# Kernel optimization log

Hardware: AMD Instinct MI355X
Metric: run time of the kernel (lower is better)

## Reference

```python
import math
import jax, jax.numpy as jnp
import numpy as np

B, CIN, COUT, K, Z, H, W = 8, 512, 512, 3, 512, 64, 64


def setup_inputs() -> dict:
    key = jax.random.key(0)
    k1, k2, k3, k4 = jax.random.split(key, 4)
    inp = {
        "input": jax.random.normal(k1, (B, CIN, H, W), dtype=jnp.float32),
        "style": jax.random.normal(k2, (B, Z), dtype=jnp.float32),
        # base conv weight: [1, out, in, k, k]
        "weight": jax.random.normal(k3, (1, COUT, CIN, K, K), dtype=jnp.float32),
        # EqualLinear modulation params (lr_mul=1, bias_init=1)
        "mod_w": jax.random.normal(k4, (CIN, Z), dtype=jnp.float32),
        "mod_b": jnp.ones((CIN,), dtype=jnp.float32),
    }
    return inp


def reference(input, style, weight, mod_w, mod_b):
    # EqualLinear: scale = 1/sqrt(z_dim), lr_mul = 1, no activation
    z_dim = mod_w.shape[1]
    mod_scale = 1.0 / math.sqrt(z_dim)
    s = style @ (mod_w * mod_scale).T + mod_b  # [B, in]

    # modulated per-sample weights: scale * base_weight * style
    in_ch, k = weight.shape[2], weight.shape[-1]
    conv_scale = 1.0 / math.sqrt(in_ch * k * k)
    w = conv_scale * weight * s[:, None, :, None, None]  # [B, out, in, k, k]

    pad = k // 2

    def conv_one(x, wb):  # x: [in, H, W], wb: [out, in, k, k]
        return jax.lax.conv_general_dilated(
            x[None], wb, window_strides=(1, 1),
            padding=[(pad, pad), (pad, pad)],
            dimension_numbers=("NCHW", "OIHW", "NCHW"),
        )[0]

    out = jax.vmap(conv_one)(input, w)  # [B, out, H, W]
    return out
```

## Files before the change

kernel.cpp:

```cpp
#include <hip/hip_runtime.h>
#include <hip/hip_bf16.h>

#define BB   8
#define CIN  512
#define COUT 512
#define ZD   512
#define HH   64
#define WW   64

#define MOD_SCALE  0.04419417382415922f
#define CONV_SCALE 0.014731391274719742f

typedef __bf16 bf16x8 __attribute__((ext_vector_type(8)));
typedef float  f32x4  __attribute__((ext_vector_type(4)));

static __device__ __forceinline__ unsigned short f32_to_bf16_rne(float f) {
    unsigned int u = __float_as_uint(f);
    u = (u + 0x7FFFu + ((u >> 16) & 1u)) >> 16;
    return (unsigned short)u;
}

__global__ void k_style(const float* __restrict__ style, const float* __restrict__ mod_w,
                        const float* __restrict__ mod_b, float* __restrict__ sconv) {
    int wid  = blockIdx.x * 4 + (threadIdx.x >> 6);
    int lane = threadIdx.x & 63;
    int b = wid >> 9;
    int i = wid & 511;
    const float4* st = (const float4*)(style + (size_t)b * ZD);
    const float4* mw = (const float4*)(mod_w + (size_t)i * ZD);
    float4 a0 = st[lane],      b0 = mw[lane];
    float4 a1 = st[lane + 64], b1 = mw[lane + 64];
    float sum = a0.x*b0.x + a0.y*b0.y + a0.z*b0.z + a0.w*b0.w
              + a1.x*b1.x + a1.y*b1.y + a1.z*b1.z + a1.w*b1.w;
    #pragma unroll
    for (int off = 32; off > 0; off >>= 1) sum += __shfl_down(sum, off);
    if (lane == 0) sconv[wid] = (sum * MOD_SCALE + mod_b[i]) * CONV_SCALE;
}

__global__ void k_scale_input(const float* __restrict__ input, const float* __restrict__ sconv,
                              unsigned short* __restrict__ xs2) {
    int i0 = blockIdx.x * 32;
    int h  = blockIdx.y;
    int b  = blockIdx.z;
    __shared__ unsigned short lds[64][40];
    #pragma unroll
    for (int r = 0; r < 8; ++r) {
        int ii = r * 4 + (threadIdx.x >> 6);
        int w  = threadIdx.x & 63;
        float v = input[(((size_t)b * CIN + i0 + ii) * HH + h) * WW + w];
        float s = sconv[b * CIN + i0 + ii];
        lds[w][ii] = f32_to_bf16_rne(v * s);
    }
    __syncthreads();
    int w = threadIdx.x >> 2, q = threadIdx.x & 3;
    int4 val = *(const int4*)&lds[w][q * 8];
    *(int4*)&xs2[(((size_t)b * HH + h) * WW + w) * CIN + i0 + q * 8] = val;
}

__global__ void k_weight(const float* __restrict__ weight, unsigned short* __restrict__ w2) {
    int t = blockIdx.x * 256 + threadIdx.x;
    int o = t >> 9, i = t & 511;
    const float* src = weight + ((size_t)o * CIN + i) * 9;
    #pragma unroll
    for (int p = 0; p < 9; ++p)
        w2[((size_t)p * COUT + o) * CIN + i] = f32_to_bf16_rne(src[p]);
}

#define PADI 40

__global__ __launch_bounds__(256, 2)
void k_conv(const unsigned short* __restrict__ xs2, const unsigned short* __restrict__ w2,
            float* __restrict__ out) {
    int y0  = blockIdx.x * 4;
    int oc0 = blockIdx.y * 64;
    int b   = blockIdx.z;
    int tid  = threadIdx.x;
    int wv   = tid >> 6;
    int lane = tid & 63;
    int lm = lane & 15, hi = lane >> 4;

    __shared__ unsigned short lds_w[9 * 64 * PADI];
    __shared__ unsigned short lds_x[6 * 66 * PADI];

    f32x4 acc[4][4];
    #pragma unroll
    for (int mt = 0; mt < 4; ++mt)
        #pragma unroll
        for (int nt = 0; nt < 4; ++nt)
            acc[mt][nt] = (f32x4){0.f, 0.f, 0.f, 0.f};

    for (int ic = 0; ic < 16; ++ic) {
        int i0 = ic * 32;
        __syncthreads();
        #pragma unroll
        for (int v = 0; v < 9; ++v) {
            int idx = v * 256 + tid;
            int po = idx >> 2;
            int q  = idx & 3;
            int p = po >> 6, o = po & 63;
            int4 val = *(const int4*)&w2[((size_t)p * COUT + oc0 + o) * CIN + i0 + q * 8];
            *(int4*)&lds_w[po * PADI + q * 8] = val;
        }
        #pragma unroll
        for (int v = 0; v < 7; ++v) {
            int idx = v * 256 + tid;
            if (idx < 1584) {
                int pr = idx >> 2;
                int q  = idx & 3;
                int rr = pr / 66, xx = pr - rr * 66;
                int hy = y0 - 1 + rr;
                int x  = xx - 1;
                int4 val = {0, 0, 0, 0};
                if ((unsigned)hy < 64u && (unsigned)x < 64u)
                    val = *(const int4*)&xs2[(((size_t)b * HH + hy) * WW + x) * CIN + i0 + q * 8];
                *(int4*)&lds_x[pr * PADI + q * 8] = val;
            }
        }
        __syncthreads();
        #pragma unroll
        for (int p = 0; p < 9; ++p) {
            int kh = p / 3, kw = p - kh * 3;
            bf16x8 afrag[4], bfrag[4];
            #pragma unroll
            for (int mt = 0; mt < 4; ++mt)
                afrag[mt] = *(const bf16x8*)&lds_w[(p * 64 + mt * 16 + lm) * PADI + 8 * hi];
            #pragma unroll
            for (int nt = 0; nt < 4; ++nt)
                bfrag[nt] = *(const bf16x8*)&lds_x[((wv + kh) * 66 + nt * 16 + lm + kw) * PADI + 8 * hi];
            #pragma unroll
            for (int mt = 0; mt < 4; ++mt)
                #pragma unroll
                for (int nt = 0; nt < 4; ++nt)
                    acc[mt][nt] = __builtin_amdgcn_mfma_f32_16x16x32_bf16(
                        afrag[mt], bfrag[nt], acc[mt][nt], 0, 0, 0);
        }
    }
    int y = y0 + wv;
    #pragma unroll
    for (int mt = 0; mt < 4; ++mt)
        #pragma unroll
        for (int nt = 0; nt < 4; ++nt)
            #pragma unroll
            for (int r = 0; r < 4; ++r) {
                int oc = oc0 + mt * 16 + hi * 4 + r;
                out[(((size_t)b * COUT + oc) * HH + y) * WW + nt * 16 + lm] = acc[mt][nt][r];
            }
}

extern "C" void kernel_launch(void* const* d_in, const int* in_sizes, int n_in,
                              void* d_out, int out_size, void* d_ws, size_t ws_size,
                              hipStream_t stream) {
    const float* input  = (const float*)d_in[0];
    const float* style  = (const float*)d_in[1];
    const float* weight = (const float*)d_in[2];
    const float* mod_w  = (const float*)d_in[3];
    const float* mod_b  = (const float*)d_in[4];
    float* out = (float*)d_out;

    const size_t xs2_bytes = (size_t)BB * HH * WW * CIN * 2;
    const size_t w2_bytes  = (size_t)9 * COUT * CIN * 2;
    const size_t need = 16384 + xs2_bytes + w2_bytes;
    if (ws_size < need) return;

    float*          sconv = (float*)d_ws;
    unsigned short* xs2   = (unsigned short*)((char*)d_ws + 16384);
    unsigned short* w2    = (unsigned short*)((char*)d_ws + 16384 + xs2_bytes);

    hipLaunchKernelGGL(k_style,       dim3(1024),      dim3(256), 0, stream, style, mod_w, mod_b, sconv);
    hipLaunchKernelGGL(k_weight,      dim3(1024),      dim3(256), 0, stream, weight, w2);
    hipLaunchKernelGGL(k_scale_input, dim3(16, 64, 8), dim3(256), 0, stream, input, sconv, xs2);
    hipLaunchKernelGGL(k_conv,        dim3(16, 8, 8),  dim3(256), 0, stream, xs2, w2, out);
}
```

Before: 182.7 us.

## Pipeline conv with direct global-to-LDS loads, padded input and pre-swizzled weights

Pads the scaled input buffer with a zeroed one-pixel border so the conv needs no bounds checks. Pre-arranges the bf16 weights into 16-byte granules matching the LDS layout. Rewrites the conv kernel to 512 threads with a 256-output-channel tile. It streams weights per tap through a 4-deep LDS ring and double-buffers input channel chunks using global_load_lds with explicit vmcnt waits and barriers, overlapping loads with MFMA work. This uses more LDS and tighter barrier-based synchronisation, which risks stalls and ordering errors if the wait counts are wrong.

```diff
diff --git a/kernel.cpp b/kernel.cpp
--- a/kernel.cpp
+++ b/kernel.cpp
@@ -37,8 +37,21 @@
     if (lane == 0) sconv[wid] = (sum * MOD_SCALE + mod_b[i]) * CONV_SCALE;
 }
 
+__global__ void k_zero_border(unsigned short* __restrict__ xs2p) {
+    int b = blockIdx.y;
+    int p = blockIdx.x * 4 + (threadIdx.x >> 6);
+    int lane = threadIdx.x & 63;
+    int h, w;
+    if (p < 66)       { h = 0;       w = p; }
+    else if (p < 132) { h = 65;      w = p - 66; }
+    else if (p < 196) { h = p - 131; w = 0; }
+    else              { h = p - 195; w = 65; }
+    int4 z = {0, 0, 0, 0};
+    *(int4*)&xs2p[((size_t)(b * 66 + h) * 66 + w) * 512 + lane * 8] = z;
+}
+
 __global__ void k_scale_input(const float* __restrict__ input, const float* __restrict__ sconv,
-                              unsigned short* __restrict__ xs2) {
+                              unsigned short* __restrict__ xs2p) {
     int i0 = blockIdx.x * 32;
     int h  = blockIdx.y;
     int b  = blockIdx.z;
@@ -54,96 +67,149 @@
     __syncthreads();
     int w = threadIdx.x >> 2, q = threadIdx.x & 3;
     int4 val = *(const int4*)&lds[w][q * 8];
-    *(int4*)&xs2[(((size_t)b * HH + h) * WW + w) * CIN + i0 + q * 8] = val;
-}
-
-__global__ void k_weight(const float* __restrict__ weight, unsigned short* __restrict__ w2) {
+    *(int4*)&xs2p[((size_t)(b * 66 + h + 1) * 66 + (w + 1)) * 512 + i0 + q * 8] = val;
+}
+
+__global__ void k_weight(const float* __restrict__ weight, unsigned short* __restrict__ w2g) {
     int t = blockIdx.x * 256 + threadIdx.x;
     int o = t >> 9, i = t & 511;
+    int c = i >> 5, g = (i >> 3) & 3, il = i & 7;
     const float* src = weight + ((size_t)o * CIN + i) * 9;
     #pragma unroll
-    for (int p = 0; p < 9; ++p)
-        w2[((size_t)p * COUT + o) * CIN + i] = f32_to_bf16_rne(src[p]);
-}
-
-#define PADI 40
-
-__global__ __launch_bounds__(256, 2)
-void k_conv(const unsigned short* __restrict__ xs2, const unsigned short* __restrict__ w2,
+    for (int p = 0; p < 9; ++p) {
+        size_t gran = ((size_t)(p * 16 + c) * 4 + g) * 512 + o;
+        w2g[gran * 8 + il] = f32_to_bf16_rne(src[p]);
+    }
+}
+
+#define WBOFF(j) ((j) * 16384)
+#define XBOFF(j) (65536 + (j) * 32768)
+
+#define GLD(srcp, ldsbyte)                                                        \
+    __builtin_amdgcn_global_load_lds(                                             \
+        (const __attribute__((address_space(1))) unsigned int*)(srcp),            \
+        (__attribute__((address_space(3))) unsigned int*)(smb + (ldsbyte)),       \
+        16, 0, 0)
+
+__global__ __launch_bounds__(512, 2)
+void k_conv(const unsigned short* __restrict__ xs2p, const unsigned short* __restrict__ w2g,
             float* __restrict__ out) {
-    int y0  = blockIdx.x * 4;
-    int oc0 = blockIdx.y * 64;
-    int b   = blockIdx.z;
-    int tid  = threadIdx.x;
-    int wv   = tid >> 6;
-    int lane = tid & 63;
-    int lm = lane & 15, hi = lane >> 4;
-
-    __shared__ unsigned short lds_w[9 * 64 * PADI];
-    __shared__ unsigned short lds_x[6 * 66 * PADI];
-
-    f32x4 acc[4][4];
-    #pragma unroll
-    for (int mt = 0; mt < 4; ++mt)
+    __shared__ unsigned short smem[65536];
+    char* smb = (char*)smem;
+
+    const int tid  = threadIdx.x;
+    const int wid  = tid >> 6, lane = tid & 63;
+    const int wm   = wid >> 2, wr   = wid & 3;
+    const int lm   = lane & 15, hi  = lane >> 4;
+    const int oc0  = blockIdx.x * 256;
+    const int y0   = blockIdx.y * 4;
+    const int b    = blockIdx.z;
+
+    const int p_lin = wid * 64 + lane;
+    const int xrow  = p_lin / 66;
+    const int xcol  = p_lin - xrow * 66;
+    const char* srcX = (const char*)xs2p;
+    if (p_lin < 396)
+        srcX += ((size_t)(b * 66 + y0 + xrow) * 66 + xcol) * 1024;
+
+    const int g0   = p_lin >> 8;
+    const int oc_l = p_lin & 255;
+    const char* pW = (const char*)w2g + ((size_t)g0 * 512 + oc0 + oc_l) * 16;
+
+    const int wdst = wid * 1024 + (lane & 63) * 16;
+
+    #pragma unroll
+    for (int k = 0; k < 4; ++k)
+        GLD(srcX + k * 16, XBOFF(0) + k * 8192 + wdst);
+    GLD(pW,                    WBOFF(0) + wdst);
+    GLD(pW + 16384,            WBOFF(0) + 8192 + wdst);
+    GLD(pW + 524288,           WBOFF(1) + wdst);
+    GLD(pW + 524288 + 16384,   WBOFF(1) + 8192 + wdst);
+    pW += 2 * 524288;
+    asm volatile("s_waitcnt vmcnt(0)" ::: "memory");
+    __builtin_amdgcn_s_barrier();
+
+    f32x4 acc[8][4];
+    #pragma unroll
+    for (int mt = 0; mt < 8; ++mt)
         #pragma unroll
         for (int nt = 0; nt < 4; ++nt)
             acc[mt][nt] = (f32x4){0.f, 0.f, 0.f, 0.f};
 
-    for (int ic = 0; ic < 16; ++ic) {
-        int i0 = ic * 32;
-        __syncthreads();
-        #pragma unroll
-        for (int v = 0; v < 9; ++v) {
-            int idx = v * 256 + tid;
-            int po = idx >> 2;
-            int q  = idx & 3;
-            int p = po >> 6, o = po & 63;
-            int4 val = *(const int4*)&w2[((size_t)p * COUT + oc0 + o) * CIN + i0 + q * 8];
-            *(int4*)&lds_w[po * PADI + q * 8] = val;
+    const int aoff = hi * 4096 + (wm * 128 + lm) * 16;
+    const int boff = hi * 8192 + (wr * 66 + lm) * 16;
+
+    int tap = 0, c = 0, tap2 = 2;
+    bf16x8 afr[4], bfr[4];
+
+    for (int ts = 0; ts < 144; ++ts) {
+        const int wsel  = ts & 3;
+        const int wsel2 = (ts + 2) & 3;
+        const bool haveW2 = (ts <= 141);
+        const int kh = tap / 3;
+        const int kw = tap - kh * 3;
+        const int ko = (kh * 66 + kw) * 16;
+
+        const char* wbase = smb + WBOFF(wsel) + aoff;
+        const char* xbase = smb + XBOFF(c & 1) + boff + ko;
+
+        if (haveW2) GLD(pW, WBOFF(wsel2) + wdst);
+        if (tap == 0 && c < 15) {
+            const char* sx = srcX + (c + 1) * 64;
+            #pragma unroll
+            for (int k = 0; k < 4; ++k)
+                GLD(sx + k * 16, XBOFF((c + 1) & 1) + k * 8192 + wdst);
         }
         #pragma unroll
-        for (int v = 0; v < 7; ++v) {
-            int idx = v * 256 + tid;
-            if (idx < 1584) {
-                int pr = idx >> 2;
-                int q  = idx & 3;
-                int rr = pr / 66, xx = pr - rr * 66;
-                int hy = y0 - 1 + rr;
-                int x  = xx - 1;
-                int4 val = {0, 0, 0, 0};
-                if ((unsigned)hy < 64u && (unsigned)x < 64u)
-                    val = *(const int4*)&xs2[(((size_t)b * HH + hy) * WW + x) * CIN + i0 + q * 8];
-                *(int4*)&lds_x[pr * PADI + q * 8] = val;
-            }
+        for (int mt = 0; mt < 4; ++mt) afr[mt] = *(const bf16x8*)(wbase + mt * 256);
+        #pragma unroll
+        for (int nt = 0; nt < 4; ++nt) bfr[nt] = *(const bf16x8*)(xbase + nt * 256);
+        __builtin_amdgcn_s_barrier();
+        __builtin_amdgcn_s_setprio(1);
+        #pragma unroll
+        for (int mt = 0; mt < 4; ++mt)
+            #pragma unroll
+            for (int nt = 0; nt < 4; ++nt)
+                acc[mt][nt] = __builtin_amdgcn_mfma_f32_16x16x32_bf16(
+                    afr[mt], bfr[nt], acc[mt][nt], 0, 0, 0);
+        __builtin_amdgcn_s_setprio(0);
+        __builtin_amdgcn_s_barrier();
+
+        if (haveW2) GLD(pW + 16384, WBOFF(wsel2) + 8192 + wdst);
+        #pragma unroll
+        for (int mt = 0; mt < 4; ++mt) afr[mt] = *(const bf16x8*)(wbase + 1024 + mt * 256);
+        __builtin_amdgcn_s_barrier();
+        __builtin_amdgcn_s_setprio(1);
+        #pragma unroll
+        for (int mt = 0; mt < 4; ++mt)
+            #pragma unroll
+            for (int nt = 0; nt < 4; ++nt)
+                acc[4 + mt][nt] = __builtin_amdgcn_mfma_f32_16x16x32_bf16(
+                    afr[mt], bfr[nt], acc[4 + mt][nt], 0, 0, 0);
+        __builtin_amdgcn_s_setprio(0);
+        if (tap == 0 && c < 15)  { asm volatile("s_waitcnt vmcnt(6)" ::: "memory"); }
+        else if (ts <= 141)      { asm volatile("s_waitcnt vmcnt(2)" ::: "memory"); }
+        else                     { asm volatile("s_waitcnt vmcnt(0)" ::: "memory"); }
+        __builtin_amdgcn_s_barrier();
+
+        if (haveW2) {
+            ++tap2;
+            if (tap2 == 9) { tap2 = 0; pW -= 127 * 32768; }
+            else           { pW += 524288; }
         }
-        __syncthreads();
-        #pragma unroll
-        for (int p = 0; p < 9; ++p) {
-            int kh = p / 3, kw = p - kh * 3;
-            bf16x8 afrag[4], bfrag[4];
-            #pragma unroll
-            for (int mt = 0; mt < 4; ++mt)
-                afrag[mt] = *(const bf16x8*)&lds_w[(p * 64 + mt * 16 + lm) * PADI + 8 * hi];
-            #pragma unroll
-            for (int nt = 0; nt < 4; ++nt)
-                bfrag[nt] = *(const bf16x8*)&lds_x[((wv + kh) * 66 + nt * 16 + lm + kw) * PADI + 8 * hi];
-            #pragma unroll
-            for (int mt = 0; mt < 4; ++mt)
-                #pragma unroll
-                for (int nt = 0; nt < 4; ++nt)
-                    acc[mt][nt] = __builtin_amdgcn_mfma_f32_16x16x32_bf16(
-                        afrag[mt], bfrag[nt], acc[mt][nt], 0, 0, 0);
-        }
+        ++tap;
+        if (tap == 9) { tap = 0; ++c; }
     }
-    int y = y0 + wv;
-    #pragma unroll
-    for (int mt = 0; mt < 4; ++mt)
+
+    const int ybase = (y0 + wr) * 64;
+    #pragma unroll
+    for (int mt = 0; mt < 8; ++mt)
         #pragma unroll
         for (int nt = 0; nt < 4; ++nt)
             #pragma unroll
             for (int r = 0; r < 4; ++r) {
-                int oc = oc0 + mt * 16 + hi * 4 + r;
-                out[(((size_t)b * COUT + oc) * HH + y) * WW + nt * 16 + lm] = acc[mt][nt][r];
+                int oc = oc0 + wm * 128 + mt * 16 + hi * 4 + r;
+                out[((size_t)(b * COUT + oc) << 12) + ybase + nt * 16 + lm] = acc[mt][nt][r];
             }
 }
 
@@ -157,17 +223,18 @@
     const float* mod_b  = (const float*)d_in[4];
     float* out = (float*)d_out;
 
-    const size_t xs2_bytes = (size_t)BB * HH * WW * CIN * 2;
-    const size_t w2_bytes  = (size_t)9 * COUT * CIN * 2;
-    const size_t need = 16384 + xs2_bytes + w2_bytes;
+    const size_t xs2p_bytes = (size_t)BB * 66 * 66 * 512 * 2;
+    const size_t w2_bytes   = (size_t)9 * 16 * 4 * 512 * 8 * 2;
+    const size_t need = 16384 + xs2p_bytes + w2_bytes;
     if (ws_size < need) return;
 
     float*          sconv = (float*)d_ws;
-    unsigned short* xs2   = (unsigned short*)((char*)d_ws + 16384);
-    unsigned short* w2    = (unsigned short*)((char*)d_ws + 16384 + xs2_bytes);
+    unsigned short* xs2p  = (unsigned short*)((char*)d_ws + 16384);
+    unsigned short* w2g   = (unsigned short*)((char*)d_ws + 16384 + xs2p_bytes);
 
     hipLaunchKernelGGL(k_style,       dim3(1024),      dim3(256), 0, stream, style, mod_w, mod_b, sconv);
-    hipLaunchKernelGGL(k_weight,      dim3(1024),      dim3(256), 0, stream, weight, w2);
-    hipLaunchKernelGGL(k_scale_input, dim3(16, 64, 8), dim3(256), 0, stream, input, sconv, xs2);
-    hipLaunchKernelGGL(k_conv,        dim3(16, 8, 8),  dim3(256), 0, stream, xs2, w2, out);
-}
+    hipLaunchKernelGGL(k_weight,      dim3(1024),      dim3(256), 0, stream, weight, w2g);
+    hipLaunchKernelGGL(k_zero_border, dim3(65, 8),     dim3(256), 0, stream, xs2p);
+    hipLaunchKernelGGL(k_scale_input, dim3(16, 64, 8), dim3(256), 0, stream, input, sconv, xs2p);
+    hipLaunchKernelGGL(k_conv,        dim3(2, 16, 8),  dim3(512), 0, stream, xs2p, w2g, out);
+}
```

Result: no change. 181.0 us (-0.9%).
